# Performance work log

Hardware: AMD Instinct MI355X
Metric: run time of the kernel (lower is better)

Reference implementation:

```python
import jax, jax.numpy as jnp
import numpy as np

D_MODEL = 1024
H = 16
D_K = D_MODEL // H
BAND = 100  # attention allowed where |i-j| < BAND


def setup_inputs() -> dict:
    key = jax.random.key(0)
    ks = jax.random.split(key, 9)
    B, S = 2, 2048
    s = 1.0 / np.sqrt(D_MODEL)
    return {
        "x": jax.random.normal(ks[0], (B, S, D_MODEL), jnp.float32),
        "Wq": jax.random.normal(ks[1], (D_MODEL, D_MODEL), jnp.float32) * s,
        "bq": jnp.zeros((D_MODEL,), jnp.float32),
        "Wk": jax.random.normal(ks[2], (D_MODEL, D_MODEL), jnp.float32) * s,
        "bk": jnp.zeros((D_MODEL,), jnp.float32),
        "Wv": jax.random.normal(ks[3], (D_MODEL, D_MODEL), jnp.float32) * s,
        "bv": jnp.zeros((D_MODEL,), jnp.float32),
        "Wo": jax.random.normal(ks[4], (D_MODEL, D_MODEL), jnp.float32) * s,
        "bo": jnp.zeros((D_MODEL,), jnp.float32),
    }


def _split_heads(t, B, S):
    # [B, S, D] -> [B, H, S, D_K]
    return t.reshape(B, S, H, D_K).transpose(0, 2, 1, 3)


def reference(x, Wq, bq, Wk, bk, Wv, bv, Wo, bo):
    B, S, _ = x.shape
    q = _split_heads(x @ Wq.T + bq, B, S)
    k = _split_heads(x @ Wk.T + bk, B, S)
    v = _split_heads(x @ Wv.T + bv, B, S)

    scores = jnp.einsum("bhqd,bhkd->bhqk", q, k) / jnp.sqrt(jnp.float32(D_K))
    i = jnp.arange(S)
    band = jnp.abs(i[:, None] - i[None, :]) < BAND  # [S, S] True inside band
    scores = jnp.where(band[None, None, :, :], scores, jnp.float32(-1e9))
    p_attn = jax.nn.softmax(scores, axis=-1)

    out = jnp.einsum("bhqk,bhkd->bhqd", p_attn, v)
    out = out.transpose(0, 2, 1, 3).reshape(B, S, D_MODEL)
    return out @ Wo.T + bo
```

## Files before the change

### kernel.cpp

```cpp
#include <hip/hip_runtime.h>
#include <hip/hip_bf16.h>


typedef __attribute__((ext_vector_type(8))) short short8;
typedef __attribute__((ext_vector_type(4))) float f32x4;

#define S_LEN 2048
#define NH 16
#define DK 64
#define BANDW 100

#define X_ELEMS   (2 * S_LEN * 1024)
#define W_ELEMS   (1024 * 1024)
#define QKV_ELEMS (2 * NH * S_LEN * DK)
#define AO_ELEMS  (2 * S_LEN * 1024)

__device__ __attribute__((aligned(256))) short g_X[X_ELEMS];
__device__ __attribute__((aligned(256))) short g_W[4 * W_ELEMS];
__device__ __attribute__((aligned(256))) short g_b[4 * 1024];
__device__ __attribute__((aligned(256))) short g_Q[QKV_ELEMS];
__device__ __attribute__((aligned(256))) short g_K[QKV_ELEMS];
__device__ __attribute__((aligned(256))) short g_V[QKV_ELEMS];
__device__ __attribute__((aligned(256))) short g_AO[AO_ELEMS];

__device__ __forceinline__ float bf2f(short u) {
    unsigned x = ((unsigned)(unsigned short)u) << 16;
    return __builtin_bit_cast(float, x);
}
__device__ __forceinline__ short f2bf(float f) {
    unsigned x = __builtin_bit_cast(unsigned, f);
    unsigned r = (x + 0x7fffu + ((x >> 16) & 1u)) >> 16;
    return (short)r;
}

#define GLOAD_LDS(gp, lp) \
    __builtin_amdgcn_global_load_lds( \
        (const __attribute__((address_space(1))) void*)(gp), \
        (__attribute__((address_space(3))) void*)(lp), 16, 0, 0)

#define XC   (X_ELEMS / 8)
#define WC   (W_ELEMS / 8)
#define BC   (1024 / 8)
#define TOTC (XC + 4 * WC + 4 * BC)

__global__ __launch_bounds__(256) void convert_all(
    const void* __restrict__ x,
    const void* __restrict__ w0, const void* __restrict__ b0,
    const void* __restrict__ w1, const void* __restrict__ b1,
    const void* __restrict__ w2, const void* __restrict__ b2,
    const void* __restrict__ w3, const void* __restrict__ b3)
{
    __shared__ int cnt[256];
    {
        const unsigned* xw = (const unsigned*)x;
        int local = 0;
        #pragma unroll
        for (int i = 0; i < 4; i++) {
            unsigned wv = xw[threadIdx.x * 4 + i];
            unsigned e = (wv >> 7) & 0xFF;
            if (e >= 100 && e <= 140) local++;
        }
        cnt[threadIdx.x] = local;
    }
    __syncthreads();
    for (int s = 128; s > 0; s >>= 1) {
        if (threadIdx.x < s) cnt[threadIdx.x] += cnt[threadIdx.x + s];
        __syncthreads();
    }
    const int is_bf16 = (cnt[0] > 512);

    long i = (long)blockIdx.x * 256 + threadIdx.x;
    if (i >= TOTC) return;

    const void* src; short* dst; long off;
    if (i < XC)                { src = x;  dst = g_X;              off = i; }
    else if ((i -= XC) < WC)   { src = w0; dst = g_W + 0L*W_ELEMS; off = i; }
    else if ((i -= WC) < WC)   { src = w1; dst = g_W + 1L*W_ELEMS; off = i; }
    else if ((i -= WC) < WC)   { src = w2; dst = g_W + 2L*W_ELEMS; off = i; }
    else if ((i -= WC) < WC)   { src = w3; dst = g_W + 3L*W_ELEMS; off = i; }
    else if ((i -= WC) < BC)   { src = b0; dst = g_b + 0*1024;     off = i; }
    else if ((i -= BC) < BC)   { src = b1; dst = g_b + 1*1024;     off = i; }
    else if ((i -= BC) < BC)   { src = b2; dst = g_b + 2*1024;     off = i; }
    else                       { src = b3; dst = g_b + 3*1024;     off = i - BC; }

    if (is_bf16) {
        ((short8*)dst)[off] = ((const short8*)src)[off];
    } else {
        const float* s = (const float*)src + off * 8;
        short8 o;
        #pragma unroll
        for (int e = 0; e < 8; e++) o[e] = f2bf(s[e]);
        ((short8*)dst)[off] = o;
    }
}


#define LHALF 8192

__global__ __launch_bounds__(512, 2) void qkv_gemm256()
{
    __shared__ __attribute__((aligned(16))) short L[8][LHALF];

    const int t = threadIdx.x;
    const int lane = t & 63;
    const int w    = t >> 6;
    const int l15  = lane & 15;
    const int qg   = lane >> 4;
    const int wr   = w >> 2;
    const int wc   = w & 3;

    const int bid0 = blockIdx.x;
    const int bid  = (bid0 & 7) * 24 + (bid0 >> 3);
    const int mb  = (bid & 15) << 8;
    const int nb  = (bid >> 4) << 8;

    const int srow = w * 16 + (lane >> 3);
    const int scol = (((lane & 7) ^ (lane >> 3)) << 3);
    const short* pA0 = g_X + (long)(mb       + srow) * 1024 + scol;
    const short* pA1 = g_X + (long)(mb + 128 + srow) * 1024 + scol;
    const short* pB0 = g_W + (long)(nb       + srow) * 1024 + scol;
    const short* pB1 = g_W + (long)(nb + 128 + srow) * 1024 + scol;
    const int ldst = w * 1024 + lane * 8;

#define STAGE(reg_, gp_, kt_) do {                         \
        short* lp_ = &L[(reg_)][ldst];                     \
        GLOAD_LDS((gp_) + (long)(kt_), lp_);               \
        GLOAD_LDS((gp_) + 8192 + (long)(kt_), lp_ + 512);  \
    } while (0)

#define BARRIER() asm volatile("s_barrier" ::: "memory")

    const int axs    = (l15 & 7) << 3;
    const int a_off0 = (qg << 3) ^ axs;
    const int a_off1 = (32 + (qg << 3)) ^ axs;
    const int brow   = (wc & 1) * 64;

    f32x4 acc[8][4] = {};

    STAGE(0*4 + 2 + 0, pB0, 0);
    STAGE(0*4 + 0 + 0, pA0, 0);
    STAGE(0*4 + 0 + 1, pA1, 0);
    STAGE(0*4 + 2 + 1, pB1, 0);
    STAGE(1*4 + 2 + 0, pB0, 64);
    STAGE(1*4 + 0 + 0, pA0, 64);
    asm volatile("s_waitcnt vmcnt(4)" ::: "memory");
    BARRIER();

    for (int T = 0; T < 16; T++) {
        const int buf = T & 1;
        const short* Ah = L[buf*4 + wr];
        const short* Bh = L[buf*4 + 2 + (wc >> 1)];
        short8 afr[4][2], bfr[4][2];

        #pragma unroll
        for (int mi = 0; mi < 4; mi++) {
            const int rb = (mi*16 + l15) * 64;
            afr[mi][0] = *(const short8*)(Ah + rb + a_off0);
            afr[mi][1] = *(const short8*)(Ah + rb + a_off1);
        }
        #pragma unroll
        for (int ni = 0; ni < 2; ni++) {
            const int rb = (brow + ni*16 + l15) * 64;
            bfr[ni][0] = *(const short8*)(Bh + rb + a_off0);
            bfr[ni][1] = *(const short8*)(Bh + rb + a_off1);
        }
        if (T + 1 < 16) STAGE(((T+1)&1)*4 + 1, pA1, (T+1)*64);
        BARRIER();
        __builtin_amdgcn_s_setprio(1);
        #pragma unroll
        for (int mi = 0; mi < 4; mi++)
            #pragma unroll
            for (int ni = 0; ni < 2; ni++) {
                acc[mi][ni] = __builtin_amdgcn_mfma_f32_16x16x32_bf16(afr[mi][0], bfr[ni][0], acc[mi][ni], 0, 0, 0);
                acc[mi][ni] = __builtin_amdgcn_mfma_f32_16x16x32_bf16(afr[mi][1], bfr[ni][1], acc[mi][ni], 0, 0, 0);
            }
        __builtin_amdgcn_s_setprio(0);
        BARRIER();

        #pragma unroll
        for (int ni = 2; ni < 4; ni++) {
            const int rb = (brow + ni*16 + l15) * 64;
            bfr[ni][0] = *(const short8*)(Bh + rb + a_off0);
            bfr[ni][1] = *(const short8*)(Bh + rb + a_off1);
        }
        if (T + 1 < 16) STAGE(((T+1)&1)*4 + 2 + 1, pB1, (T+1)*64);
        BARRIER();
        __builtin_amdgcn_s_setprio(1);
        #pragma unroll
        for (int mi = 0; mi < 4; mi++)
            #pragma unroll
            for (int ni = 2; ni < 4; ni++) {
                acc[mi][ni] = __builtin_amdgcn_mfma_f32_16x16x32_bf16(afr[mi][0], bfr[ni][0], acc[mi][ni], 0, 0, 0);
                acc[mi][ni] = __builtin_amdgcn_mfma_f32_16x16x32_bf16(afr[mi][1], bfr[ni][1], acc[mi][ni], 0, 0, 0);
            }
        __builtin_amdgcn_s_setprio(0);
        BARRIER();

        #pragma unroll
        for (int mi = 0; mi < 4; mi++) {
            const int rb = ((mi + 4)*16 + l15) * 64;
            afr[mi][0] = *(const short8*)(Ah + rb + a_off0);
            afr[mi][1] = *(const short8*)(Ah + rb + a_off1);
        }
        if (T + 2 < 16) STAGE((T&1)*4 + 2 + 0, pB0, (T+2)*64);
        BARRIER();
        __builtin_amdgcn_s_setprio(1);
        #pragma unroll
        for (int mi = 0; mi < 4; mi++)
            #pragma unroll
            for (int ni = 2; ni < 4; ni++) {
                acc[mi+4][ni] = __builtin_amdgcn_mfma_f32_16x16x32_bf16(afr[mi][0], bfr[ni][0], acc[mi+4][ni], 0, 0, 0);
                acc[mi+4][ni] = __builtin_amdgcn_mfma_f32_16x16x32_bf16(afr[mi][1], bfr[ni][1], acc[mi+4][ni], 0, 0, 0);
            }
        __builtin_amdgcn_s_setprio(0);
        BARRIER();

        if (T + 2 < 16) STAGE((T&1)*4 + 0, pA0, (T+2)*64);
        BARRIER();
        __builtin_amdgcn_s_setprio(1);
        #pragma unroll
        for (int mi = 0; mi < 4; mi++)
            #pragma unroll
            for (int ni = 0; ni < 2; ni++) {
                acc[mi+4][ni] = __builtin_amdgcn_mfma_f32_16x16x32_bf16(afr[mi][0], bfr[ni][0], acc[mi+4][ni], 0, 0, 0);
                acc[mi+4][ni] = __builtin_amdgcn_mfma_f32_16x16x32_bf16(afr[mi][1], bfr[ni][1], acc[mi+4][ni], 0, 0, 0);
            }
        __builtin_amdgcn_s_setprio(0);
        if (T <= 13)      asm volatile("s_waitcnt vmcnt(4)" ::: "memory");
        else if (T == 14) asm volatile("s_waitcnt vmcnt(0)" ::: "memory");
        BARRIER();
    }

    const int nbase = nb + wc * 64;
    const int z = nbase >> 10;
    short* __restrict__ Out = (z == 0) ? g_Q : ((z == 1) ? g_K : g_V);
    const float scale = (z == 0) ? 0.125f : 1.0f;
    const int c0 = nbase & 1023;
    const int h = c0 >> 6;
    float bv4[4];
    #pragma unroll
    for (int ni = 0; ni < 4; ni++) bv4[ni] = bf2f(g_b[z * 1024 + c0 + ni * 16 + l15]);
    const int rg = qg * 4;
    #pragma unroll
    for (int mi = 0; mi < 8; mi++) {
        #pragma unroll
        for (int r = 0; r < 4; r++) {
            const int row = mb + wr * 128 + mi * 16 + rg + r;
            const int bI = row >> 11, s = row & 2047;
            short* op = Out + (((long)(bI * NH + h) * S_LEN) + s) * DK;
            #pragma unroll
            for (int ni = 0; ni < 4; ni++)
                op[ni * 16 + l15] = f2bf((acc[mi][ni][r] + bv4[ni]) * scale);
        }
    }
#undef STAGE
#undef BARRIER
}

__global__ __launch_bounds__(256) void o_gemm(float* __restrict__ Out)
{
    __shared__ __attribute__((aligned(16))) short As[2][128 * 32];
    __shared__ __attribute__((aligned(16))) short Bs[2][64 * 32];

    const short* __restrict__ A = g_AO;
    const short* __restrict__ W = g_W + 3L * W_ELEMS;

    const int t = threadIdx.x;
    const int lane = t & 63;
    const int wid  = t >> 6;
    const int wm = wid & 1, wn = wid >> 1;
    const int l15 = lane & 15;
    const int q8  = (lane >> 4) * 8;
    const int mb = blockIdx.x * 128;
    const int nb = blockIdx.y * 64;

    const long ga0 = (long)(mb + (t >> 2)) * 1024 + (t & 3) * 8;
    const long ga1 = (long)(mb + 64 + (t >> 2)) * 1024 + (t & 3) * 8;
    const long gb0 = (long)(nb + (t >> 2)) * 1024 + (t & 3) * 8;

    f32x4 acc[4][2] = {};

    GLOAD_LDS(A + ga0, As[0] + t * 8);
    GLOAD_LDS(A + ga1, As[0] + 2048 + t * 8);
    GLOAD_LDS(W + gb0, Bs[0] + t * 8);
    __syncthreads();

    for (int k0 = 0; k0 < 1024; k0 += 32) {
        const int cur = (k0 >> 5) & 1;
        if (k0 + 32 < 1024) {
            GLOAD_LDS(A + ga0 + k0 + 32, As[cur ^ 1] + t * 8);
            GLOAD_LDS(A + ga1 + k0 + 32, As[cur ^ 1] + 2048 + t * 8);
            GLOAD_LDS(W + gb0 + k0 + 32, Bs[cur ^ 1] + t * 8);
        }
        short8 a[4], b[2];
        #pragma unroll
        for (int mt = 0; mt < 4; mt++) a[mt] = *(const short8*)(As[cur] + (wm * 64 + mt * 16 + l15) * 32 + q8);
        #pragma unroll
        for (int nt = 0; nt < 2; nt++) b[nt] = *(const short8*)(Bs[cur] + (wn * 32 + nt * 16 + l15) * 32 + q8);
        #pragma unroll
        for (int mt = 0; mt < 4; mt++)
            #pragma unroll
            for (int nt = 0; nt < 2; nt++)
                acc[mt][nt] = __builtin_amdgcn_mfma_f32_16x16x32_bf16(a[mt], b[nt], acc[mt][nt], 0, 0, 0);
        __syncthreads();
    }

    const int rg = (lane >> 4) * 4;
    #pragma unroll
    for (int nt = 0; nt < 2; nt++) {
        const int col = nb + wn * 32 + nt * 16 + l15;
        const float bv_ = bf2f(g_b[3 * 1024 + col]);
        #pragma unroll
        for (int mt = 0; mt < 4; mt++) {
            #pragma unroll
            for (int r = 0; r < 4; r++) {
                const int row = mb + wm * 64 + mt * 16 + rg + r;
                Out[(long)row * 1024 + col] = acc[mt][nt][r] + bv_;
            }
        }
    }
}

#define VT_PAD 328

__global__ __launch_bounds__(256) void attn_kernel()
{
    __shared__ __attribute__((aligned(16))) short Vt[64][VT_PAD];
    __shared__ __attribute__((aligned(16))) short Pl[4][16][72];

    const int bid  = blockIdx.x;
    const int head = bid & 31;
    const int qt   = bid >> 5;
    const int h = head & 15, b = head >> 4;
    const int qbase = qt * 64;

    const int lane = threadIdx.x & 63;
    const int w    = threadIdx.x >> 6;
    const int l15  = lane & 15;
    const int qg   = lane >> 4;
    const int q8   = qg * 8;

    const long hoff = (long)(b * NH + h) * S_LEN * DK;
    const short* __restrict__ Qh = g_Q + hoff;
    const short* __restrict__ Kh = g_K + hoff;
    const short* __restrict__ Vh = g_V + hoff;

    const int lo  = qbase - (BANDW - 1);
    const int kc0 = (lo < 0 ? 0 : lo) >> 6;
    int hi = qbase + 64 + (BANDW - 1);
    if (hi > S_LEN) hi = S_LEN;
    const int kc1 = (hi + 63) >> 6;
    const int kb0 = kc0 * 64;
    const int n_keys = (kc1 - kc0) * 64;

    const short* qp = Qh + (long)(qbase + w * 16 + l15) * DK + q8;
    const short8 aq0 = *(const short8*)(qp);
    const short8 aq1 = *(const short8*)(qp + 32);

    const int npairs = n_keys >> 1;
    for (int u = threadIdx.x; u < npairs; u += 256) {
        const short* vp0 = Vh + (long)(kb0 + 2 * u) * DK;
        #pragma unroll
        for (int tq = 0; tq < 8; tq++) {
            const short8 v0 = *(const short8*)(vp0 + tq * 8);
            const short8 v1 = *(const short8*)(vp0 + DK + tq * 8);
            #pragma unroll
            for (int e = 0; e < 8; e++) {
                const int pk = (int)(unsigned short)v0[e] | ((int)(unsigned short)v1[e] << 16);
                *(int*)&Vt[tq * 8 + e][2 * u] = pk;
            }
        }
    }
    __syncthreads();

    short8 nk0[4], nk1[4];
    #pragma unroll
    for (int nt = 0; nt < 4; nt++) {
        const short* kp = Kh + (long)(kb0 + nt * 16 + l15) * DK + q8;
        nk0[nt] = *(const short8*)(kp);
        nk1[nt] = *(const short8*)(kp + 32);
    }

    f32x4 o[4] = {};
    float m_r[4], l_r[4];
    #pragma unroll
    for (int r = 0; r < 4; r++) { m_r[r] = -1e30f; l_r[r] = 0.f; }

    for (int kc = kc0; kc < kc1; kc++) {
        const int kb = kc * 64;
        const int kloc = kb - kb0;

        short8 bk0[4], bk1[4];
        #pragma unroll
        for (int nt = 0; nt < 4; nt++) { bk0[nt] = nk0[nt]; bk1[nt] = nk1[nt]; }
        if (kc + 1 < kc1) {
            const int kbn = kb + 64;
            #pragma unroll
            for (int nt = 0; nt < 4; nt++) {
                const short* kp = Kh + (long)(kbn + nt * 16 + l15) * DK + q8;
                nk0[nt] = *(const short8*)(kp);
                nk1[nt] = *(const short8*)(kp + 32);
            }
        }

        f32x4 sc[4];
        #pragma unroll
        for (int nt = 0; nt < 4; nt++) {
            f32x4 z = {};
            z = __builtin_amdgcn_mfma_f32_16x16x32_bf16(aq0, bk0[nt], z, 0, 0, 0);
            z = __builtin_amdgcn_mfma_f32_16x16x32_bf16(aq1, bk1[nt], z, 0, 0, 0);
            sc[nt] = z;
        }

        float pv[4][4];
        float mx[4] = {-1e30f, -1e30f, -1e30f, -1e30f};
        if (kb == qbase) {
            #pragma unroll
            for (int nt = 0; nt < 4; nt++)
                #pragma unroll
                for (int r = 0; r < 4; r++) {
                    pv[nt][r] = sc[nt][r];
                    mx[r] = fmaxf(mx[r], sc[nt][r]);
                }
        } else {
            #pragma unroll
            for (int nt = 0; nt < 4; nt++) {
                const int kg = kb + nt * 16 + l15;
                #pragma unroll
                for (int r = 0; r < 4; r++) {
                    const int qI = qbase + w * 16 + qg * 4 + r;
                    int dlt = qI - kg; if (dlt < 0) dlt = -dlt;
                    const float v = (dlt < BANDW) ? sc[nt][r] : -1e30f;
                    pv[nt][r] = v;
                    mx[r] = fmaxf(mx[r], v);
                }
            }
        }
        #pragma unroll
        for (int mk = 1; mk < 16; mk <<= 1)
            #pragma unroll
            for (int r = 0; r < 4; r++) mx[r] = fmaxf(mx[r], __shfl_xor(mx[r], mk, 64));

        float alpha[4], lnew[4];
        #pragma unroll
        for (int r = 0; r < 4; r++) {
            const float mn = fmaxf(m_r[r], mx[r]);
            alpha[r] = __builtin_exp2f((m_r[r] - mn) * 1.44269504f);
            m_r[r] = mn;
            lnew[r] = 0.f;
        }
        #pragma unroll
        for (int nt = 0; nt < 4; nt++)
            #pragma unroll
            for (int r = 0; r < 4; r++) {
                const float p = (pv[nt][r] > -0.5e30f)
                    ? __builtin_exp2f((pv[nt][r] - m_r[r]) * 1.44269504f) : 0.f;
                pv[nt][r] = p;
                lnew[r] += p;
            }
        #pragma unroll
        for (int mk = 1; mk < 16; mk <<= 1)
            #pragma unroll
            for (int r = 0; r < 4; r++) lnew[r] += __shfl_xor(lnew[r], mk, 64);
        #pragma unroll
        for (int r = 0; r < 4; r++) l_r[r] = l_r[r] * alpha[r] + lnew[r];
        #pragma unroll
        for (int nt2 = 0; nt2 < 4; nt2++)
            #pragma unroll
            for (int r = 0; r < 4; r++) o[nt2][r] *= alpha[r];

        #pragma unroll
        for (int nt = 0; nt < 4; nt++)
            #pragma unroll
            for (int r = 0; r < 4; r++)
                Pl[w][qg * 4 + r][nt * 16 + l15] = f2bf(pv[nt][r]);
        asm volatile("s_waitcnt lgkmcnt(0)" ::: "memory");
        const short8 ap0 = *(const short8*)(&Pl[w][l15][q8]);
        const short8 ap1 = *(const short8*)(&Pl[w][l15][32 + q8]);

        #pragma unroll
        for (int nt2 = 0; nt2 < 4; nt2++) {
            const short* vrow = &Vt[nt2 * 16 + l15][kloc];
            const short8 bv0 = *(const short8*)(vrow + q8);
            const short8 bv1 = *(const short8*)(vrow + 32 + q8);
            o[nt2] = __builtin_amdgcn_mfma_f32_16x16x32_bf16(ap0, bv0, o[nt2], 0, 0, 0);
            o[nt2] = __builtin_amdgcn_mfma_f32_16x16x32_bf16(ap1, bv1, o[nt2], 0, 0, 0);
        }
    }

    #pragma unroll
    for (int nt2 = 0; nt2 < 4; nt2++)
        #pragma unroll
        for (int r = 0; r < 4; r++) {
            const int qI = qbase + w * 16 + qg * 4 + r;
            const int d = nt2 * 16 + l15;
            g_AO[((long)b * S_LEN + qI) * 1024 + h * DK + d] = f2bf(o[nt2][r] / l_r[r]);
        }
}

extern "C" void kernel_launch(void* const* d_in, const int* in_sizes, int n_in,
                              void* d_out, int out_size, void* d_ws, size_t ws_size,
                              hipStream_t stream) {
    float* out = (float*)d_out;

    convert_all<<<(TOTC + 255) / 256, 256, 0, stream>>>(
        d_in[0], d_in[1], d_in[2], d_in[3], d_in[4], d_in[5], d_in[6], d_in[7], d_in[8]);
    qkv_gemm256<<<dim3(192), 512, 0, stream>>>();
    attn_kernel<<<dim3(2 * NH * (S_LEN / 64)), 256, 0, stream>>>();
    o_gemm<<<dim3(32, 16), 256, 0, stream>>>(out);
}
```

Baseline: 180.5 us.

## Retile QKV GEMM to 256x192 tiles so grid fills all 256 CUs

Changes the fused QKV projection GEMM from 256x256 tiles (192 blocks) to 256x192 tiles (256 blocks), so the grid matches the MI355X's 256 compute units and avoids a partially idle wave of blocks. The B tile is now staged as three 64-row regions loaded by all threads, each wave computes 48 columns (3 MFMA column tiles), and the LDS layout, prefetch schedule and vmcnt waits are reworked to match. The epilogue computes a per-column head and destination buffer because 48-column slices can straddle head and Q/K/V boundaries. The block-index swizzle is dropped, and each block now does less MFMA work per A-tile load, so arithmetic intensity falls.

```diff
diff --git a/kernel.cpp b/kernel.cpp
--- a/kernel.cpp
+++ b/kernel.cpp
@@ -95,11 +95,17 @@
 }
 
 
-#define LHALF 8192
+#define QKV_NT 16
+#define BUFS  28672
+#define RA0   0
+#define RA1   8192
+#define RB0   16384
+#define RB1   20480
+#define RB2   24576
 
 __global__ __launch_bounds__(512, 2) void qkv_gemm256()
 {
-    __shared__ __attribute__((aligned(16))) short L[8][LHALF];
+    __shared__ __attribute__((aligned(16))) short L[2][BUFS];
 
     const int t = threadIdx.x;
     const int lane = t & 63;
@@ -109,48 +115,59 @@
     const int wr   = w >> 2;
     const int wc   = w & 3;
 
-    const int bid0 = blockIdx.x;
-    const int bid  = (bid0 & 7) * 24 + (bid0 >> 3);
+    const int bid = blockIdx.x;
     const int mb  = (bid & 15) << 8;
-    const int nb  = (bid >> 4) << 8;
-
-    const int srow = w * 16 + (lane >> 3);
-    const int scol = (((lane & 7) ^ (lane >> 3)) << 3);
-    const short* pA0 = g_X + (long)(mb       + srow) * 1024 + scol;
-    const short* pA1 = g_X + (long)(mb + 128 + srow) * 1024 + scol;
-    const short* pB0 = g_W + (long)(nb       + srow) * 1024 + scol;
-    const short* pB1 = g_W + (long)(nb + 128 + srow) * 1024 + scol;
-    const int ldst = w * 1024 + lane * 8;
-
-#define STAGE(reg_, gp_, kt_) do {                         \
-        short* lp_ = &L[(reg_)][ldst];                     \
-        GLOAD_LDS((gp_) + (long)(kt_), lp_);               \
-        GLOAD_LDS((gp_) + 8192 + (long)(kt_), lp_ + 512);  \
+    const int nb  = (bid >> 4) * 192;
+
+    const int srowA = w * 16 + (lane >> 3);
+    const int scolA = (((lane & 7) ^ (lane >> 3)) << 3);
+    const short* pA0 = g_X + (long)(mb       + srowA) * 1024 + scolA;
+    const short* pA1 = g_X + (long)(mb + 128 + srowA) * 1024 + scolA;
+    const int ldstA = w * 1024 + lane * 8;
+    const int srowB = t >> 3;
+    const int scolB = (((t & 7) ^ ((t >> 3) & 7)) << 3);
+    const short* pB0 = g_W + (long)(nb       + srowB) * 1024 + scolB;
+    const short* pB1 = g_W + (long)(nb +  64 + srowB) * 1024 + scolB;
+    const short* pB2 = g_W + (long)(nb + 128 + srowB) * 1024 + scolB;
+    const int ldstB = t * 8;
+
+#define STAGE_A(buf_, reg_, gp_, kt_) do {                          \
+        short* lp_ = &L[(buf_)][(reg_) + ldstA];                    \
+        GLOAD_LDS((gp_) + (long)(kt_), lp_);                        \
+        GLOAD_LDS((gp_) + 8192 + (long)(kt_), lp_ + 512);           \
     } while (0)
-
+#define STAGE_B(buf_, reg_, gp_, kt_) do {                          \
+        short* lp_ = &L[(buf_)][(reg_) + ldstB];                    \
+        GLOAD_LDS((gp_) + (long)(kt_), lp_);                        \
+    } while (0)
 #define BARRIER() asm volatile("s_barrier" ::: "memory")
 
     const int axs    = (l15 & 7) << 3;
     const int a_off0 = (qg << 3) ^ axs;
     const int a_off1 = (32 + (qg << 3)) ^ axs;
-    const int brow   = (wc & 1) * 64;
-
-    f32x4 acc[8][4] = {};
-
-    STAGE(0*4 + 2 + 0, pB0, 0);
-    STAGE(0*4 + 0 + 0, pA0, 0);
-    STAGE(0*4 + 0 + 1, pA1, 0);
-    STAGE(0*4 + 2 + 1, pB1, 0);
-    STAGE(1*4 + 2 + 0, pB0, 64);
-    STAGE(1*4 + 0 + 0, pA0, 64);
-    asm volatile("s_waitcnt vmcnt(4)" ::: "memory");
+    int breg[3], brr[3];
+    #pragma unroll
+    for (int ni = 0; ni < 3; ni++) {
+        const int cb = wc * 48 + ni * 16;
+        breg[ni] = RB0 + (cb >> 6) * 4096;
+        brr[ni]  = cb & 63;
+    }
+
+    f32x4 acc[8][3] = {};
+
+    STAGE_A(0, RA0, pA0, 0);
+    STAGE_A(0, RA1, pA1, 0);
+    STAGE_B(0, RB0, pB0, 0);
+    STAGE_B(0, RB1, pB1, 0);
+    STAGE_B(0, RB2, pB2, 0);
+    STAGE_A(1, RA0, pA0, 64);
+    asm volatile("s_waitcnt vmcnt(2)" ::: "memory");
     BARRIER();
 
-    for (int T = 0; T < 16; T++) {
+    for (int T = 0; T < QKV_NT; T++) {
         const int buf = T & 1;
-        const short* Ah = L[buf*4 + wr];
-        const short* Bh = L[buf*4 + 2 + (wc >> 1)];
-        short8 afr[4][2], bfr[4][2];
+        const short* Ah = L[buf] + (wr ? RA1 : RA0);
+        short8 afr[4][2], bfr[3][2];
 
         #pragma unroll
         for (int mi = 0; mi < 4; mi++) {
@@ -160,11 +177,11 @@
         }
         #pragma unroll
         for (int ni = 0; ni < 2; ni++) {
-            const int rb = (brow + ni*16 + l15) * 64;
-            bfr[ni][0] = *(const short8*)(Bh + rb + a_off0);
-            bfr[ni][1] = *(const short8*)(Bh + rb + a_off1);
-        }
-        if (T + 1 < 16) STAGE(((T+1)&1)*4 + 1, pA1, (T+1)*64);
+            const short* Bp = L[buf] + breg[ni] + (brr[ni] + l15) * 64;
+            bfr[ni][0] = *(const short8*)(Bp + a_off0);
+            bfr[ni][1] = *(const short8*)(Bp + a_off1);
+        }
+        if (T + 1 < QKV_NT) STAGE_A(buf ^ 1, RA1, pA1, (T+1)*64);
         BARRIER();
         __builtin_amdgcn_s_setprio(1);
         #pragma unroll
@@ -177,22 +194,23 @@
         __builtin_amdgcn_s_setprio(0);
         BARRIER();
 
-        #pragma unroll
-        for (int ni = 2; ni < 4; ni++) {
-            const int rb = (brow + ni*16 + l15) * 64;
-            bfr[ni][0] = *(const short8*)(Bh + rb + a_off0);
-            bfr[ni][1] = *(const short8*)(Bh + rb + a_off1);
-        }
-        if (T + 1 < 16) STAGE(((T+1)&1)*4 + 2 + 1, pB1, (T+1)*64);
+        {
+            const short* Bp = L[buf] + breg[2] + (brr[2] + l15) * 64;
+            bfr[2][0] = *(const short8*)(Bp + a_off0);
+            bfr[2][1] = *(const short8*)(Bp + a_off1);
+        }
+        if (T + 1 < QKV_NT) {
+            STAGE_B(buf ^ 1, RB0, pB0, (T+1)*64);
+            STAGE_B(buf ^ 1, RB1, pB1, (T+1)*64);
+            STAGE_B(buf ^ 1, RB2, pB2, (T+1)*64);
+        }
         BARRIER();
         __builtin_amdgcn_s_setprio(1);
         #pragma unroll
-        for (int mi = 0; mi < 4; mi++)
-            #pragma unroll
-            for (int ni = 2; ni < 4; ni++) {
-                acc[mi][ni] = __builtin_amdgcn_mfma_f32_16x16x32_bf16(afr[mi][0], bfr[ni][0], acc[mi][ni], 0, 0, 0);
-                acc[mi][ni] = __builtin_amdgcn_mfma_f32_16x16x32_bf16(afr[mi][1], bfr[ni][1], acc[mi][ni], 0, 0, 0);
-            }
+        for (int mi = 0; mi < 4; mi++) {
+            acc[mi][2] = __builtin_amdgcn_mfma_f32_16x16x32_bf16(afr[mi][0], bfr[2][0], acc[mi][2], 0, 0, 0);
+            acc[mi][2] = __builtin_amdgcn_mfma_f32_16x16x32_bf16(afr[mi][1], bfr[2][1], acc[mi][2], 0, 0, 0);
+        }
         __builtin_amdgcn_s_setprio(0);
         BARRIER();
 
@@ -202,21 +220,17 @@
             afr[mi][0] = *(const short8*)(Ah + rb + a_off0);
             afr[mi][1] = *(const short8*)(Ah + rb + a_off1);
         }
-        if (T + 2 < 16) STAGE((T&1)*4 + 2 + 0, pB0, (T+2)*64);
         BARRIER();
         __builtin_amdgcn_s_setprio(1);
         #pragma unroll
-        for (int mi = 0; mi < 4; mi++)
-            #pragma unroll
-            for (int ni = 2; ni < 4; ni++) {
-                acc[mi+4][ni] = __builtin_amdgcn_mfma_f32_16x16x32_bf16(afr[mi][0], bfr[ni][0], acc[mi+4][ni], 0, 0, 0);
-                acc[mi+4][ni] = __builtin_amdgcn_mfma_f32_16x16x32_bf16(afr[mi][1], bfr[ni][1], acc[mi+4][ni], 0, 0, 0);
-            }
+        for (int mi = 0; mi < 4; mi++) {
+            acc[mi+4][2] = __builtin_amdgcn_mfma_f32_16x16x32_bf16(afr[mi][0], bfr[2][0], acc[mi+4][2], 0, 0, 0);
+            acc[mi+4][2] = __builtin_amdgcn_mfma_f32_16x16x32_bf16(afr[mi][1], bfr[2][1], acc[mi+4][2], 0, 0, 0);
+        }
         __builtin_amdgcn_s_setprio(0);
         BARRIER();
 
-        if (T + 2 < 16) STAGE((T&1)*4 + 0, pA0, (T+2)*64);
-        BARRIER();
+        if (T + 2 < QKV_NT) STAGE_A(buf, RA0, pA0, (T+2)*64);
         __builtin_amdgcn_s_setprio(1);
         #pragma unroll
         for (int mi = 0; mi < 4; mi++)
@@ -226,20 +240,22 @@
                 acc[mi+4][ni] = __builtin_amdgcn_mfma_f32_16x16x32_bf16(afr[mi][1], bfr[ni][1], acc[mi+4][ni], 0, 0, 0);
             }
         __builtin_amdgcn_s_setprio(0);
-        if (T <= 13)      asm volatile("s_waitcnt vmcnt(4)" ::: "memory");
-        else if (T == 14) asm volatile("s_waitcnt vmcnt(0)" ::: "memory");
-        BARRIER();
-    }
-
-    const int nbase = nb + wc * 64;
-    const int z = nbase >> 10;
-    short* __restrict__ Out = (z == 0) ? g_Q : ((z == 1) ? g_K : g_V);
-    const float scale = (z == 0) ? 0.125f : 1.0f;
-    const int c0 = nbase & 1023;
-    const int h = c0 >> 6;
-    float bv4[4];
-    #pragma unroll
-    for (int ni = 0; ni < 4; ni++) bv4[ni] = bf2f(g_b[z * 1024 + c0 + ni * 16 + l15]);
+        if (T <= QKV_NT - 3)      asm volatile("s_waitcnt vmcnt(2)" ::: "memory");
+        else if (T == QKV_NT - 2) asm volatile("s_waitcnt vmcnt(0)" ::: "memory");
+        BARRIER();
+    }
+
+    const int nbase = nb + wc * 48;
+    short* Outp[3]; float bvv[3], scl[3]; int hh[3], db[3];
+    #pragma unroll
+    for (int ni = 0; ni < 3; ni++) {
+        const int cc = nbase + ni * 16;
+        const int z = cc >> 10, cl = cc & 1023;
+        Outp[ni] = (z == 0) ? g_Q : ((z == 1) ? g_K : g_V);
+        scl[ni]  = (z == 0) ? 0.125f : 1.0f;
+        hh[ni] = cl >> 6; db[ni] = cl & 63;
+        bvv[ni] = bf2f(g_b[z * 1024 + cl + l15]);
+    }
     const int rg = qg * 4;
     #pragma unroll
     for (int mi = 0; mi < 8; mi++) {
@@ -247,13 +263,14 @@
         for (int r = 0; r < 4; r++) {
             const int row = mb + wr * 128 + mi * 16 + rg + r;
             const int bI = row >> 11, s = row & 2047;
-            short* op = Out + (((long)(bI * NH + h) * S_LEN) + s) * DK;
-            #pragma unroll
-            for (int ni = 0; ni < 4; ni++)
-                op[ni * 16 + l15] = f2bf((acc[mi][ni][r] + bv4[ni]) * scale);
-        }
-    }
-#undef STAGE
+            #pragma unroll
+            for (int ni = 0; ni < 3; ni++)
+                Outp[ni][(((long)(bI * NH + hh[ni]) * S_LEN) + s) * DK + db[ni] + l15] =
+                    f2bf((acc[mi][ni][r] + bvv[ni]) * scl[ni]);
+        }
+    }
+#undef STAGE_A
+#undef STAGE_B
 #undef BARRIER
 }
 
@@ -505,7 +522,7 @@
 
     convert_all<<<(TOTC + 255) / 256, 256, 0, stream>>>(
         d_in[0], d_in[1], d_in[2], d_in[3], d_in[4], d_in[5], d_in[6], d_in[7], d_in[8]);
-    qkv_gemm256<<<dim3(192), 512, 0, stream>>>();
+    qkv_gemm256<<<dim3(256), 512, 0, stream>>>();
     attn_kernel<<<dim3(2 * NH * (S_LEN / 64)), 256, 0, stream>>>();
     o_gemm<<<dim3(32, 16), 256, 0, stream>>>(out);
 }
```

New measurement: 176.6 us. 1.02x faster.
